# Kernel optimization log

Measured on AMD Instinct MI355X. Metric: run time of the kernel, lower is better.

Reference implementation:

```python
import jax, jax.numpy as jnp
import numpy as np

N = 100000
E = 200000
SD = 128   # structural_dim
CD = 768   # chemical_dim


def _linear_params(key, fan_in, fan_out):
    kw, kb = jax.random.split(key)
    bound = 1.0 / np.sqrt(fan_in)
    W = jax.random.uniform(kw, (fan_in, fan_out), jnp.float32, -bound, bound)
    b = jax.random.uniform(kb, (fan_out,), jnp.float32, -bound, bound)
    return W, b


def setup_inputs() -> dict:
    key = jax.random.key(0)
    ks = jax.random.split(key, 12)
    z = jax.random.normal(ks[0], (N, SD), jnp.float32)
    chemistry = jax.random.normal(ks[1], (N, CD), jnp.float32)
    edge = jax.random.randint(ks[2], (E, 2), 0, N, jnp.int64)
    smiles_mask = jax.random.randint(ks[3], (N,), 0, 2, jnp.int32)
    # structural_mlp: SD -> SD//2 -> 1
    sw1, sb1 = _linear_params(ks[4], SD, SD // 2)
    sw2, sb2 = _linear_params(ks[5], SD // 2, 1)
    # chemical_mlp: CD -> CD//4 -> 1
    cw1, cb1 = _linear_params(ks[6], CD, CD // 4)
    cw2, cb2 = _linear_params(ks[7], CD // 4, 1)
    # combined_mlp: SD+CD -> SD -> 1
    mw1, mb1 = _linear_params(ks[8], SD + CD, SD)
    mw2, mb2 = _linear_params(ks[9], SD, 1)
    path_weights = jnp.ones((3,), jnp.float32) / 3.0
    return dict(z=z, chemistry=chemistry, edge=edge, smiles_mask=smiles_mask,
                sw1=sw1, sb1=sb1, sw2=sw2, sb2=sb2,
                cw1=cw1, cb1=cb1, cw2=cw2, cb2=cb2,
                mw1=mw1, mb1=mb1, mw2=mw2, mb2=mb2,
                path_weights=path_weights)


def reference(z, chemistry, edge, smiles_mask,
              sw1, sb1, sw2, sb2,
              cw1, cb1, cw2, cb2,
              mw1, mb1, mw2, mb2,
              path_weights):
    src, dst = edge[:, 0], edge[:, 1]
    # per-edge gathers + elementwise products
    structural_prod = z[src] * z[dst]                    # [E, SD]
    chemical_prod = chemistry[src] * chemistry[dst]      # [E, CD]
    # three small MLPs (dropout is identity in eval mode)
    score_structural = (jax.nn.relu(structural_prod @ sw1 + sb1) @ sw2 + sb2)[:, 0]
    score_chemical = (jax.nn.relu(chemical_prod @ cw1 + cb1) @ cw2 + cb2)[:, 0]
    combined_prod = jnp.concatenate([structural_prod, chemical_prod], axis=-1)  # [E, SD+CD]
    score_combined = (jax.nn.relu(combined_prod @ mw1 + mb1) @ mw2 + mb2)[:, 0]
    # fixed learned path weights (use_gating=False)
    w = jax.nn.softmax(path_weights)
    scores = w[0] * score_structural + w[1] * score_chemical + w[2] * score_combined
    # fall back to structural-only score where chemistry is missing on either end
    mask = smiles_mask.astype(z.dtype)
    both_valid = mask[src] * mask[dst]
    return jnp.where(both_valid > 0.5, scores, score_structural)  # [E]
```

## Files before the change

### kernel.cpp

```cpp
#include <hip/hip_runtime.h>


typedef float    f32x4 __attribute__((ext_vector_type(4)));
typedef _Float16 f16x8 __attribute__((ext_vector_type(8)));
typedef _Float16 f16x4 __attribute__((ext_vector_type(4)));

#define E_EDGES 200000
#define KSTEPS  28
#define NOUT    384
#define PTOT    (KSTEPS * NOUT * 32)
#define PANEL   (NOUT * 32)

#define WS_WH    0
#define WS_B1    688128
#define WS_W2    (688128 + 1536)
#define WS_CONST (688128 + 3072)

__global__ __launch_bounds__(256) void prep_kernel(
    const float* __restrict__ sw1, const float* __restrict__ sb1,
    const float* __restrict__ sw2, const float* __restrict__ sb2,
    const float* __restrict__ cw1, const float* __restrict__ cb1,
    const float* __restrict__ cw2, const float* __restrict__ cb2,
    const float* __restrict__ mw1, const float* __restrict__ mb1,
    const float* __restrict__ mw2, const float* __restrict__ mb2,
    const float* __restrict__ pw,  const int* __restrict__ edge_i32,
    _Float16* __restrict__ wh,
    float* __restrict__ b1cat, float* __restrict__ w2cat,
    float* __restrict__ consts)
{
  const int idx = blockIdx.x * 256 + threadIdx.x;
  if (idx < PTOT) {
    const int p  = idx / PANEL;
    const int r  = idx % PANEL;
    const int n  = r >> 5;
    const int kk = r & 31;
    const int k  = p * 32 + kk;
    float v;
    if (n < 64)       v = (k < 128)  ? sw1[k * 64 + n] : 0.0f;
    else if (n < 256) v = (k >= 128) ? cw1[(size_t)(k - 128) * 192 + (n - 64)] : 0.0f;
    else              v = mw1[(size_t)k * 128 + (n - 256)];
    wh[idx] = (_Float16)v;
  } else if (idx < PTOT + NOUT) {
    const int j = idx - PTOT;
    float b, w;
    if (j < 64)       { b = sb1[j];       w = sw2[j]; }
    else if (j < 256) { b = cb1[j - 64];  w = cw2[j - 64]; }
    else              { b = mb1[j - 256]; w = mw2[j - 256]; }
    b1cat[j] = b;
    w2cat[j] = w;
  } else if (idx == PTOT + NOUT) {
    const float p0 = pw[0], p1 = pw[1], p2 = pw[2];
    const float mx = fmaxf(p0, fmaxf(p1, p2));
    const float e0 = __expf(p0 - mx), e1 = __expf(p1 - mx), e2 = __expf(p2 - mx);
    const float inv = 1.0f / (e0 + e1 + e2);
    const float w0 = e0 * inv, w1 = e1 * inv, w2v = e2 * inv;
    consts[0] = w0; consts[1] = w1; consts[2] = w2v;
    consts[3] = w0 * sb2[0] + w1 * cb2[0] + w2v * mb2[0];
    consts[4] = sb2[0];
    unsigned o = 0;
    for (int i = 0; i < 64; ++i) o |= (unsigned)edge_i32[2 * i + 1];
    consts[5] = (o == 0u) ? 1.0f : 0.0f;
  }
}

#define FMA2(ACC, AH, AL, B)                                              \
  ACC = __builtin_amdgcn_mfma_f32_16x16x32_f16(AH, B, ACC, 0, 0, 0);      \
  ACC = __builtin_amdgcn_mfma_f32_16x16x32_f16(AL, B, ACC, 0, 0, 0);

__global__ __launch_bounds__(256, 3) void decoder_main(
    const float* __restrict__ z, const float* __restrict__ chem,
    const int* __restrict__ edge, const int* __restrict__ mask,
    const _Float16* __restrict__ wh,
    const float* __restrict__ b1cat, const float* __restrict__ w2cat,
    const float* __restrict__ consts, float* __restrict__ out)
{
  __shared__ _Float16 Ash[2][4][32][40];
  __shared__ int   srcL[32];
  __shared__ int   dstL[32];
  __shared__ float validL[32];
  __shared__ float scoreW[4][32];

  const int tid  = threadIdx.x;
  const int lane = tid & 63;
  const int wv   = tid >> 6;
  const int li   = lane & 15;
  const int q    = lane >> 4;
  const int q8   = q << 3;
  const int base = blockIdx.x * 32;

  if (tid < 32) {
    const int e = base + tid;
    int s_, d_;
    if (consts[5] > 0.5f) { s_ = edge[4 * e]; d_ = edge[4 * e + 2]; }
    else                  { s_ = edge[2 * e]; d_ = edge[2 * e + 1]; }
    srcL[tid] = s_;
    dstL[tid] = d_;
    validL[tid] = (mask[s_] != 0 && mask[d_] != 0) ? 1.0f : 0.0f;
  }
  __syncthreads();

  const int m  = tid >> 3;
  const int kc = (tid & 7) << 2;
  const float* zs = z    + (size_t)srcL[m] * 128 + kc;
  const float* zd = z    + (size_t)dstL[m] * 128 + kc;
  const float* cs = chem + (size_t)srcL[m] * 768 + kc;
  const float* cd = chem + (size_t)dstL[m] * 768 + kc;

  const int loff = li * 32 + q8;
  const int tS  = wv;
  const int tH0 = 4 + 3 * wv;
  const int tC0 = 16 + 2 * wv;

#define GLOAD(T, GA, GB)                                    \
  if ((T) < 4) {                                            \
    GA = *(const f32x4*)(zs + (T) * 32);                    \
    GB = *(const f32x4*)(zd + (T) * 32);                    \
  } else {                                                  \
    GA = *(const f32x4*)(cs + ((T) - 4) * 32);              \
    GB = *(const f32x4*)(cd + ((T) - 4) * 32);              \
  }

#define ISSUE(S, GA, GB)                                    \
  { GA = *(const f32x4*)(cs + (size_t)(S) * 32);            \
    GB = *(const f32x4*)(cd + (size_t)(S) * 32); }

#define STAGE(BUF, PA, PB)                                  \
  {                                                         \
    f16x4 h_, l_;                                           \
    _Pragma("unroll")                                       \
    for (int j = 0; j < 4; ++j) {                           \
      const float p_ = (PA)[j] * (PB)[j];                   \
      const _Float16 hh = (_Float16)p_;                     \
      h_[j] = hh;                                           \
      l_[j] = (_Float16)(p_ - (float)hh);                   \
    }                                                       \
    *(f16x4*)&Ash[0][BUF][m][kc] = h_;                      \
    *(f16x4*)&Ash[1][BUF][m][kc] = l_;                      \
  }

#define AFRAGS(BC, A0H, A0L, A1H, A1L)                      \
  A0H = *(const f16x8*)&Ash[0][BC][li][q8];                 \
  A0L = *(const f16x8*)&Ash[1][BC][li][q8];                 \
  A1H = *(const f16x8*)&Ash[0][BC][16 + li][q8];            \
  A1L = *(const f16x8*)&Ash[1][BC][16 + li][q8];

  const float w0c = consts[0], w1c = consts[1], w2c = consts[2];

  float part[2][4];
#pragma unroll
  for (int mt = 0; mt < 2; ++mt)
#pragma unroll
    for (int r = 0; r < 4; ++r) part[mt][r] = 0.0f;

#define RETIRE(ACC, TI, MT, WVALID, WINVALID)                              \
  {                                                                        \
    const int col = (TI) * 16 + li;                                        \
    const float b1 = b1cat[col];                                           \
    const float w2 = w2cat[col];                                           \
    _Pragma("unroll")                                                      \
    for (int r = 0; r < 4; ++r) {                                          \
      const float vld = validL[(MT) * 16 + q * 4 + r];                     \
      const float a = (WINVALID) + vld * ((WVALID) - (WINVALID));          \
      part[MT][r] += a * fmaxf((ACC)[r] + b1, 0.0f) * w2;                  \
    }                                                                      \
  }

  f32x4 g0a, g0b, g1a, g1b, gxa, gxb, gya, gyb;
  GLOAD(0, g0a, g0b)
  GLOAD(1, g1a, g1b)
  GLOAD(2, gxa, gxb)
  GLOAD(3, gya, gyb)
  STAGE(0, g0a, g0b)
  STAGE(1, g1a, g1b)
  __syncthreads();

  f32x4 accS[2], accC[2][2];
  accS[0] = (f32x4){0.f, 0.f, 0.f, 0.f};
  accS[1] = (f32x4){0.f, 0.f, 0.f, 0.f};
#pragma unroll
  for (int t = 0; t < 2; ++t) {
    accC[t][0] = (f32x4){0.f, 0.f, 0.f, 0.f};
    accC[t][1] = (f32x4){0.f, 0.f, 0.f, 0.f};
  }

#define STEP_A(S, GA, GB)                                           \
  {                                                                 \
    const int bc = (S) & 3;                                         \
    f16x8 a0h, a0l, a1h, a1l;                                       \
    AFRAGS(bc, a0h, a0l, a1h, a1l)                                  \
    const _Float16* bu = wh + (size_t)(S) * PANEL + loff;           \
    const f16x8 bS  = *(const f16x8*)(bu + tS * 512);               \
    const f16x8 bC0 = *(const f16x8*)(bu + tC0 * 512);              \
    const f16x8 bC1 = *(const f16x8*)(bu + tC0 * 512 + 512);        \
    FMA2(accS[0],    a0h, a0l, bS)                                  \
    FMA2(accS[1],    a1h, a1l, bS)                                  \
    FMA2(accC[0][0], a0h, a0l, bC0)                                 \
    FMA2(accC[0][1], a1h, a1l, bC0)                                 \
    FMA2(accC[1][0], a0h, a0l, bC1)                                 \
    FMA2(accC[1][1], a1h, a1l, bC1)                                 \
    STAGE((bc + 2) & 3, GA, GB)                                     \
    ISSUE((S), GA, GB)                                              \
  }

  STEP_A(0, gxa, gxb)
  STEP_A(1, gya, gyb)
  __syncthreads();
  STEP_A(2, gxa, gxb)
  STEP_A(3, gya, gyb)
  __syncthreads();

  RETIRE(accS[0], tS, 0, w0c, 1.0f)
  RETIRE(accS[1], tS, 1, w0c, 1.0f)

  f32x4 accH[3][2];
#pragma unroll
  for (int t = 0; t < 3; ++t) {
    accH[t][0] = (f32x4){0.f, 0.f, 0.f, 0.f};
    accH[t][1] = (f32x4){0.f, 0.f, 0.f, 0.f};
  }

#define STEP_B(S, GA, GB, DO_STAGE, DO_ISSUE)                       \
  {                                                                 \
    const int bc = (S) & 3;                                         \
    f16x8 a0h, a0l, a1h, a1l;                                       \
    AFRAGS(bc, a0h, a0l, a1h, a1l)                                  \
    const _Float16* bu = wh + (size_t)(S) * PANEL + loff;           \
    const f16x8 bH0 = *(const f16x8*)(bu + tH0 * 512);              \
    const f16x8 bH1 = *(const f16x8*)(bu + tH0 * 512 + 512);        \
    const f16x8 bH2 = *(const f16x8*)(bu + tH0 * 512 + 1024);       \
    const f16x8 bC0 = *(const f16x8*)(bu + tC0 * 512);              \
    const f16x8 bC1 = *(const f16x8*)(bu + tC0 * 512 + 512);        \
    FMA2(accH[0][0], a0h, a0l, bH0)                                 \
    FMA2(accH[0][1], a1h, a1l, bH0)                                 \
    FMA2(accH[1][0], a0h, a0l, bH1)                                 \
    FMA2(accH[1][1], a1h, a1l, bH1)                                 \
    FMA2(accH[2][0], a0h, a0l, bH2)                                 \
    FMA2(accH[2][1], a1h, a1l, bH2)                                 \
    FMA2(accC[0][0], a0h, a0l, bC0)                                 \
    FMA2(accC[0][1], a1h, a1l, bC0)                                 \
    FMA2(accC[1][0], a0h, a0l, bC1)                                 \
    FMA2(accC[1][1], a1h, a1l, bC1)                                 \
    if (DO_STAGE) STAGE((bc + 2) & 3, GA, GB)                       \
    if (DO_ISSUE) ISSUE((S), GA, GB)                                \
  }

  for (int u = 2; u < 12; ++u) {
    STEP_B(2 * u,     gxa, gxb, true, true)
    STEP_B(2 * u + 1, gya, gyb, true, true)
    __syncthreads();
  }
  STEP_B(24, gxa, gxb, true,  false)
  STEP_B(25, gya, gyb, true,  false)
  __syncthreads();
  STEP_B(26, gxa, gxb, false, false)
  STEP_B(27, gya, gyb, false, false)

#pragma unroll
  for (int t = 0; t < 3; ++t) {
    RETIRE(accH[t][0], tH0 + t, 0, w1c, 0.0f)
    RETIRE(accH[t][1], tH0 + t, 1, w1c, 0.0f)
  }
#pragma unroll
  for (int t = 0; t < 2; ++t) {
    RETIRE(accC[t][0], tC0 + t, 0, w2c, 0.0f)
    RETIRE(accC[t][1], tC0 + t, 1, w2c, 0.0f)
  }

#pragma unroll
  for (int mt = 0; mt < 2; ++mt) {
#pragma unroll
    for (int r = 0; r < 4; ++r) {
      float vv = part[mt][r];
      vv += __shfl_xor(vv, 1);
      vv += __shfl_xor(vv, 2);
      vv += __shfl_xor(vv, 4);
      vv += __shfl_xor(vv, 8);
      part[mt][r] = vv;
    }
  }
  if (li == 0) {
#pragma unroll
    for (int mt = 0; mt < 2; ++mt)
#pragma unroll
      for (int r = 0; r < 4; ++r)
        scoreW[wv][mt * 16 + q * 4 + r] = part[mt][r];
  }
  __syncthreads();

  if (tid < 32) {
    const float s4 = scoreW[0][tid] + scoreW[1][tid] + scoreW[2][tid] + scoreW[3][tid];
    const float c3 = consts[3], c4 = consts[4];
    out[base + tid] = s4 + c4 + validL[tid] * (c3 - c4);
  }
}

extern "C" void kernel_launch(void* const* d_in, const int* in_sizes, int n_in,
                              void* d_out, int out_size, void* d_ws, size_t ws_size,
                              hipStream_t stream)
{
  const float* z    = (const float*)d_in[0];
  const float* chem = (const float*)d_in[1];
  const int*   edge = (const int*)d_in[2];
  const int*   mask = (const int*)d_in[3];
  const float* sw1  = (const float*)d_in[4];
  const float* sb1  = (const float*)d_in[5];
  const float* sw2  = (const float*)d_in[6];
  const float* sb2  = (const float*)d_in[7];
  const float* cw1  = (const float*)d_in[8];
  const float* cb1  = (const float*)d_in[9];
  const float* cw2  = (const float*)d_in[10];
  const float* cb2  = (const float*)d_in[11];
  const float* mw1  = (const float*)d_in[12];
  const float* mb1  = (const float*)d_in[13];
  const float* mw2  = (const float*)d_in[14];
  const float* mb2  = (const float*)d_in[15];
  const float* pw   = (const float*)d_in[16];

  char* ws = (char*)d_ws;
  _Float16* wh  = (_Float16*)(ws + WS_WH);
  float* b1cat  = (float*)(ws + WS_B1);
  float* w2cat  = (float*)(ws + WS_W2);
  float* consts = (float*)(ws + WS_CONST);

  const int prep_tasks  = PTOT + NOUT + 64;
  const int prep_blocks = (prep_tasks + 255) / 256;
  prep_kernel<<<prep_blocks, 256, 0, stream>>>(
      sw1, sb1, sw2, sb2, cw1, cb1, cw2, cb2, mw1, mb1, mw2, mb2, pw, edge,
      wh, b1cat, w2cat, consts);

  decoder_main<<<E_EDGES / 32, 256, 0, stream>>>(
      z, chem, edge, mask, wh, b1cat, w2cat, consts, (float*)d_out);
}
```

Before: 722.1 us.

## Split 32-edge tile across 8 waves, one 16-row M tile each

Doubles the block to 512 threads so each wave handles a single 16-row M tile instead of both. This halves the per-wave accumulator registers and per-thread gather width (float2 instead of float4), aiming for more resident waves and better latency hiding. The cost is that every B-fragment load from the weight panel is now issued by twice as many waves, and per-thread memory requests get smaller.

New measurement: 909.9 us. 26.0% more time.

```diff
diff --git a/kernel.cpp b/kernel.cpp
--- a/kernel.cpp
+++ b/kernel.cpp
@@ -2,8 +2,9 @@
 
 
 typedef float    f32x4 __attribute__((ext_vector_type(4)));
+typedef float    f32x2 __attribute__((ext_vector_type(2)));
 typedef _Float16 f16x8 __attribute__((ext_vector_type(8)));
-typedef _Float16 f16x4 __attribute__((ext_vector_type(4)));
+typedef _Float16 f16x2 __attribute__((ext_vector_type(2)));
 
 #define E_EDGES 200000
 #define KSTEPS  28
@@ -67,7 +68,7 @@
   ACC = __builtin_amdgcn_mfma_f32_16x16x32_f16(AH, B, ACC, 0, 0, 0);      \
   ACC = __builtin_amdgcn_mfma_f32_16x16x32_f16(AL, B, ACC, 0, 0, 0);
 
-__global__ __launch_bounds__(256, 3) void decoder_main(
+__global__ __launch_bounds__(512, 5) void decoder_main(
     const float* __restrict__ z, const float* __restrict__ chem,
     const int* __restrict__ edge, const int* __restrict__ mask,
     const _Float16* __restrict__ wh,
@@ -78,11 +79,13 @@
   __shared__ int   srcL[32];
   __shared__ int   dstL[32];
   __shared__ float validL[32];
-  __shared__ float scoreW[4][32];
+  __shared__ float scoreW[8][32];
 
   const int tid  = threadIdx.x;
   const int lane = tid & 63;
   const int wv   = tid >> 6;
+  const int g    = wv & 3;
+  const int mrow = (wv >> 2) << 4;
   const int li   = lane & 15;
   const int q    = lane >> 4;
   const int q8   = q << 3;
@@ -99,73 +102,69 @@
   }
   __syncthreads();
 
-  const int m  = tid >> 3;
-  const int kc = (tid & 7) << 2;
+  const int m  = tid >> 4;
+  const int kc = (tid & 15) << 1;
   const float* zs = z    + (size_t)srcL[m] * 128 + kc;
   const float* zd = z    + (size_t)dstL[m] * 128 + kc;
   const float* cs = chem + (size_t)srcL[m] * 768 + kc;
   const float* cd = chem + (size_t)dstL[m] * 768 + kc;
 
   const int loff = li * 32 + q8;
-  const int tS  = wv;
-  const int tH0 = 4 + 3 * wv;
-  const int tC0 = 16 + 2 * wv;
+  const int tS  = g;
+  const int tH0 = 4 + 3 * g;
+  const int tC0 = 16 + 2 * g;
 
 #define GLOAD(T, GA, GB)                                    \
   if ((T) < 4) {                                            \
-    GA = *(const f32x4*)(zs + (T) * 32);                    \
-    GB = *(const f32x4*)(zd + (T) * 32);                    \
+    GA = *(const f32x2*)(zs + (T) * 32);                    \
+    GB = *(const f32x2*)(zd + (T) * 32);                    \
   } else {                                                  \
-    GA = *(const f32x4*)(cs + ((T) - 4) * 32);              \
-    GB = *(const f32x4*)(cd + ((T) - 4) * 32);              \
+    GA = *(const f32x2*)(cs + ((T) - 4) * 32);              \
+    GB = *(const f32x2*)(cd + ((T) - 4) * 32);              \
   }
 
 #define ISSUE(S, GA, GB)                                    \
-  { GA = *(const f32x4*)(cs + (size_t)(S) * 32);            \
-    GB = *(const f32x4*)(cd + (size_t)(S) * 32); }
+  { GA = *(const f32x2*)(cs + (size_t)(S) * 32);            \
+    GB = *(const f32x2*)(cd + (size_t)(S) * 32); }
 
 #define STAGE(BUF, PA, PB)                                  \
   {                                                         \
-    f16x4 h_, l_;                                           \
+    f16x2 h_, l_;                                           \
     _Pragma("unroll")                                       \
-    for (int j = 0; j < 4; ++j) {                           \
+    for (int j = 0; j < 2; ++j) {                           \
       const float p_ = (PA)[j] * (PB)[j];                   \
       const _Float16 hh = (_Float16)p_;                     \
       h_[j] = hh;                                           \
       l_[j] = (_Float16)(p_ - (float)hh);                   \
     }                                                       \
-    *(f16x4*)&Ash[0][BUF][m][kc] = h_;                      \
-    *(f16x4*)&Ash[1][BUF][m][kc] = l_;                      \
-  }
-
-#define AFRAGS(BC, A0H, A0L, A1H, A1L)                      \
-  A0H = *(const f16x8*)&Ash[0][BC][li][q8];                 \
-  A0L = *(const f16x8*)&Ash[1][BC][li][q8];                 \
-  A1H = *(const f16x8*)&Ash[0][BC][16 + li][q8];            \
-  A1L = *(const f16x8*)&Ash[1][BC][16 + li][q8];
+    *(f16x2*)&Ash[0][BUF][m][kc] = h_;                      \
+    *(f16x2*)&Ash[1][BUF][m][kc] = l_;                      \
+  }
+
+#define AFRAGS(BC, AH, AL)                                  \
+  AH = *(const f16x8*)&Ash[0][BC][mrow + li][q8];           \
+  AL = *(const f16x8*)&Ash[1][BC][mrow + li][q8];
 
   const float w0c = consts[0], w1c = consts[1], w2c = consts[2];
 
-  float part[2][4];
-#pragma unroll
-  for (int mt = 0; mt < 2; ++mt)
-#pragma unroll
-    for (int r = 0; r < 4; ++r) part[mt][r] = 0.0f;
-
-#define RETIRE(ACC, TI, MT, WVALID, WINVALID)                              \
+  float part[4];
+#pragma unroll
+  for (int r = 0; r < 4; ++r) part[r] = 0.0f;
+
+#define RETIRE(ACC, TI, WVALID, WINVALID)                                  \
   {                                                                        \
     const int col = (TI) * 16 + li;                                        \
     const float b1 = b1cat[col];                                           \
     const float w2 = w2cat[col];                                           \
     _Pragma("unroll")                                                      \
     for (int r = 0; r < 4; ++r) {                                          \
-      const float vld = validL[(MT) * 16 + q * 4 + r];                     \
+      const float vld = validL[mrow + q * 4 + r];                          \
       const float a = (WINVALID) + vld * ((WVALID) - (WINVALID));          \
-      part[MT][r] += a * fmaxf((ACC)[r] + b1, 0.0f) * w2;                  \
+      part[r] += a * fmaxf((ACC)[r] + b1, 0.0f) * w2;                      \
     }                                                                      \
   }
 
-  f32x4 g0a, g0b, g1a, g1b, gxa, gxb, gya, gyb;
+  f32x2 g0a, g0b, g1a, g1b, gxa, gxb, gya, gyb;
   GLOAD(0, g0a, g0b)
   GLOAD(1, g1a, g1b)
   GLOAD(2, gxa, gxb)
@@ -174,30 +173,23 @@
   STAGE(1, g1a, g1b)
   __syncthreads();
 
-  f32x4 accS[2], accC[2][2];
-  accS[0] = (f32x4){0.f, 0.f, 0.f, 0.f};
-  accS[1] = (f32x4){0.f, 0.f, 0.f, 0.f};
-#pragma unroll
-  for (int t = 0; t < 2; ++t) {
-    accC[t][0] = (f32x4){0.f, 0.f, 0.f, 0.f};
-    accC[t][1] = (f32x4){0.f, 0.f, 0.f, 0.f};
-  }
+  f32x4 accS, accC[2];
+  accS = (f32x4){0.f, 0.f, 0.f, 0.f};
+  accC[0] = (f32x4){0.f, 0.f, 0.f, 0.f};
+  accC[1] = (f32x4){0.f, 0.f, 0.f, 0.f};
 
 #define STEP_A(S, GA, GB)                                           \
   {                                                                 \
     const int bc = (S) & 3;                                         \
-    f16x8 a0h, a0l, a1h, a1l;                                       \
-    AFRAGS(bc, a0h, a0l, a1h, a1l)                                  \
+    f16x8 ah, al;                                                   \
+    AFRAGS(bc, ah, al)                                              \
     const _Float16* bu = wh + (size_t)(S) * PANEL + loff;           \
     const f16x8 bS  = *(const f16x8*)(bu + tS * 512);               \
     const f16x8 bC0 = *(const f16x8*)(bu + tC0 * 512);              \
     const f16x8 bC1 = *(const f16x8*)(bu + tC0 * 512 + 512);        \
-    FMA2(accS[0],    a0h, a0l, bS)                                  \
-    FMA2(accS[1],    a1h, a1l, bS)                                  \
-    FMA2(accC[0][0], a0h, a0l, bC0)                                 \
-    FMA2(accC[0][1], a1h, a1l, bC0)                                 \
-    FMA2(accC[1][0], a0h, a0l, bC1)                                 \
-    FMA2(accC[1][1], a1h, a1l, bC1)                                 \
+    FMA2(accS,    ah, al, bS)                                       \
+    FMA2(accC[0], ah, al, bC0)                                      \
+    FMA2(accC[1], ah, al, bC1)                                      \
     STAGE((bc + 2) & 3, GA, GB)                                     \
     ISSUE((S), GA, GB)                                              \
   }
@@ -209,37 +201,28 @@
   STEP_A(3, gya, gyb)
   __syncthreads();
 
-  RETIRE(accS[0], tS, 0, w0c, 1.0f)
-  RETIRE(accS[1], tS, 1, w0c, 1.0f)
-
-  f32x4 accH[3][2];
-#pragma unroll
-  for (int t = 0; t < 3; ++t) {
-    accH[t][0] = (f32x4){0.f, 0.f, 0.f, 0.f};
-    accH[t][1] = (f32x4){0.f, 0.f, 0.f, 0.f};
-  }
+  RETIRE(accS, tS, w0c, 1.0f)
+
+  f32x4 accH[3];
+#pragma unroll
+  for (int t = 0; t < 3; ++t) accH[t] = (f32x4){0.f, 0.f, 0.f, 0.f};
 
 #define STEP_B(S, GA, GB, DO_STAGE, DO_ISSUE)                       \
   {                                                                 \
     const int bc = (S) & 3;                                         \
-    f16x8 a0h, a0l, a1h, a1l;                                       \
-    AFRAGS(bc, a0h, a0l, a1h, a1l)                                  \
+    f16x8 ah, al;                                                   \
+    AFRAGS(bc, ah, al)                                              \
     const _Float16* bu = wh + (size_t)(S) * PANEL + loff;           \
     const f16x8 bH0 = *(const f16x8*)(bu + tH0 * 512);              \
     const f16x8 bH1 = *(const f16x8*)(bu + tH0 * 512 + 512);        \
     const f16x8 bH2 = *(const f16x8*)(bu + tH0 * 512 + 1024);       \
     const f16x8 bC0 = *(const f16x8*)(bu + tC0 * 512);              \
     const f16x8 bC1 = *(const f16x8*)(bu + tC0 * 512 + 512);        \
-    FMA2(accH[0][0], a0h, a0l, bH0)                                 \
-    FMA2(accH[0][1], a1h, a1l, bH0)                                 \
-    FMA2(accH[1][0], a0h, a0l, bH1)                                 \
-    FMA2(accH[1][1], a1h, a1l, bH1)                                 \
-    FMA2(accH[2][0], a0h, a0l, bH2)                                 \
-    FMA2(accH[2][1], a1h, a1l, bH2)                                 \
-    FMA2(accC[0][0], a0h, a0l, bC0)                                 \
-    FMA2(accC[0][1], a1h, a1l, bC0)                                 \
-    FMA2(accC[1][0], a0h, a0l, bC1)                                 \
-    FMA2(accC[1][1], a1h, a1l, bC1)                                 \
+    FMA2(accH[0], ah, al, bH0)                                      \
+    FMA2(accH[1], ah, al, bH1)                                      \
+    FMA2(accH[2], ah, al, bH2)                                      \
+    FMA2(accC[0], ah, al, bC0)                                      \
+    FMA2(accC[1], ah, al, bC1)                                      \
     if (DO_STAGE) STAGE((bc + 2) & 3, GA, GB)                       \
     if (DO_ISSUE) ISSUE((S), GA, GB)                                \
   }
@@ -257,38 +240,33 @@
 
 #pragma unroll
   for (int t = 0; t < 3; ++t) {
-    RETIRE(accH[t][0], tH0 + t, 0, w1c, 0.0f)
-    RETIRE(accH[t][1], tH0 + t, 1, w1c, 0.0f)
+    RETIRE(accH[t], tH0 + t, w1c, 0.0f)
   }
 #pragma unroll
   for (int t = 0; t < 2; ++t) {
-    RETIRE(accC[t][0], tC0 + t, 0, w2c, 0.0f)
-    RETIRE(accC[t][1], tC0 + t, 1, w2c, 0.0f)
-  }
-
-#pragma unroll
-  for (int mt = 0; mt < 2; ++mt) {
-#pragma unroll
-    for (int r = 0; r < 4; ++r) {
-      float vv = part[mt][r];
-      vv += __shfl_xor(vv, 1);
-      vv += __shfl_xor(vv, 2);
-      vv += __shfl_xor(vv, 4);
-      vv += __shfl_xor(vv, 8);
-      part[mt][r] = vv;
-    }
+    RETIRE(accC[t], tC0 + t, w2c, 0.0f)
+  }
+
+#pragma unroll
+  for (int r = 0; r < 4; ++r) {
+    float vv = part[r];
+    vv += __shfl_xor(vv, 1);
+    vv += __shfl_xor(vv, 2);
+    vv += __shfl_xor(vv, 4);
+    vv += __shfl_xor(vv, 8);
+    part[r] = vv;
   }
   if (li == 0) {
 #pragma unroll
-    for (int mt = 0; mt < 2; ++mt)
-#pragma unroll
-      for (int r = 0; r < 4; ++r)
-        scoreW[wv][mt * 16 + q * 4 + r] = part[mt][r];
+    for (int r = 0; r < 4; ++r)
+      scoreW[wv][mrow + q * 4 + r] = part[r];
   }
   __syncthreads();
 
   if (tid < 32) {
-    const float s4 = scoreW[0][tid] + scoreW[1][tid] + scoreW[2][tid] + scoreW[3][tid];
+    const int w0 = (tid >> 4) << 2;
+    const float s4 = scoreW[w0][tid] + scoreW[w0 + 1][tid] +
+                     scoreW[w0 + 2][tid] + scoreW[w0 + 3][tid];
     const float c3 = consts[3], c4 = consts[4];
     out[base + tid] = s4 + c4 + validL[tid] * (c3 - c4);
   }
@@ -328,6 +306,6 @@
       sw1, sb1, sw2, sb2, cw1, cb1, cw2, cb2, mw1, mb1, mw2, mb2, pw, edge,
       wh, b1cat, w2cat, consts);
 
-  decoder_main<<<E_EDGES / 32, 256, 0, stream>>>(
+  decoder_main<<<E_EDGES / 32, 512, 0, stream>>>(
       z, chem, edge, mask, wh, b1cat, w2cat, consts, (float*)d_out);
 }
```
